# Kernel tuning notes

Hardware: AMD Instinct MI355X
Metric: run time of the kernel (lower is better)

The kernel has to match this reference:

```python
import jax, jax.numpy as jnp
import numpy as np

H_IMG = 128; W_IMG = 128
TANFOVX = 0.5; TANFOVY = 0.5
SCALE_MOD = 1.0
C0 = 0.28209479177387814
C1 = 0.4886025119029199
C2 = (1.0925484305920792, -1.0925484305920792, 0.31539156525252005, -1.0925484305920792, 0.5462742152960396)
C3 = (-0.5900435899266435, 2.890611442640554, -0.4570457994644658, 0.3731763325901154, -0.4570457994644658, 1.445305721320277, -0.5900435899266435)


def quat_to_rot(q):
    q = q / jnp.linalg.norm(q, axis=-1, keepdims=True)
    r, x, y, z = q[..., 0], q[..., 1], q[..., 2], q[..., 3]
    row0 = jnp.stack([1 - 2 * (y * y + z * z), 2 * (x * y - r * z), 2 * (x * z + r * y)], -1)
    row1 = jnp.stack([2 * (x * y + r * z), 1 - 2 * (x * x + z * z), 2 * (y * z - r * x)], -1)
    row2 = jnp.stack([2 * (x * z - r * y), 2 * (y * z + r * x), 1 - 2 * (x * x + y * y)], -1)
    return jnp.stack([row0, row1, row2], -2)  # [P,3,3]


def eval_sh(sh, d):
    # sh: [P,16,3], d: [P,3] unit view directions -> RGB per gaussian (degree 3)
    x, y, z = d[:, 0:1], d[:, 1:2], d[:, 2:3]
    res = C0 * sh[:, 0]
    res = res - C1 * y * sh[:, 1] + C1 * z * sh[:, 2] - C1 * x * sh[:, 3]
    xx, yy, zz = x * x, y * y, z * z
    xy, yz, xz = x * y, y * z, x * z
    res = (res + C2[0] * xy * sh[:, 4] + C2[1] * yz * sh[:, 5]
           + C2[2] * (2 * zz - xx - yy) * sh[:, 6] + C2[3] * xz * sh[:, 7]
           + C2[4] * (xx - yy) * sh[:, 8])
    res = (res + C3[0] * y * (3 * xx - yy) * sh[:, 9] + C3[1] * xy * z * sh[:, 10]
           + C3[2] * y * (4 * zz - xx - yy) * sh[:, 11]
           + C3[3] * z * (2 * zz - 3 * xx - 3 * yy) * sh[:, 12]
           + C3[4] * x * (4 * zz - xx - yy) * sh[:, 13]
           + C3[5] * z * (xx - yy) * sh[:, 14] + C3[6] * x * (xx - 3 * yy) * sh[:, 15])
    return jnp.maximum(res + 0.5, 0.0)


def _render_one(means, sh, opac, scales, rots, bg, target, view, proj, campos):
    P = means.shape[0]
    fx = W_IMG / (2.0 * TANFOVX)
    fy = H_IMG / (2.0 * TANFOVY)
    ones = jnp.ones((P, 1), means.dtype)
    xyz1 = jnp.concatenate([means, ones], axis=1)
    hom = xyz1 @ proj.T                                   # [P,4]
    p_w = 1.0 / (hom[:, 3] + 1e-7)
    p_proj = hom[:, :3] * p_w[:, None]
    p_view = xyz1 @ view.T
    depth = p_view[:, 2]
    in_front = depth > 0.2

    # 3D covariance: Sigma = R diag(s) (R diag(s))^T
    R = quat_to_rot(rots)
    M = R * (scales * SCALE_MOD)[:, None, :]
    Sigma = M @ jnp.swapaxes(M, 1, 2)                     # [P,3,3]

    # EWA Jacobian -> 2D covariance
    tz = depth
    txc = jnp.clip(p_view[:, 0] / tz, -1.3 * TANFOVX, 1.3 * TANFOVX) * tz
    tyc = jnp.clip(p_view[:, 1] / tz, -1.3 * TANFOVY, 1.3 * TANFOVY) * tz
    zp = jnp.zeros_like(tz)
    J = jnp.stack([jnp.stack([fx / tz, zp, -fx * txc / (tz * tz)], -1),
                   jnp.stack([zp, fy / tz, -fy * tyc / (tz * tz)], -1)], -2)  # [P,2,3]
    T = J @ view[:3, :3]
    cov2d = T @ Sigma @ jnp.swapaxes(T, 1, 2)             # [P,2,2]
    c00 = cov2d[:, 0, 0] + 0.3
    c11 = cov2d[:, 1, 1] + 0.3
    c01 = cov2d[:, 0, 1]
    det = c00 * c11 - c01 * c01
    valid = in_front & (det > 1e-12)
    inv_det = 1.0 / jnp.where(det > 1e-12, det, 1.0)
    conic = jnp.stack([c11 * inv_det, -c01 * inv_det, c00 * inv_det], -1)
    mid = 0.5 * (c00 + c11)
    lam = mid + jnp.sqrt(jnp.maximum(mid * mid - det, 0.1))
    radii = jnp.where(valid, jnp.ceil(3.0 * jnp.sqrt(lam)), 0.0)

    # NDC -> pixel centers
    px = ((p_proj[:, 0] + 1.0) * W_IMG - 1.0) * 0.5
    py = ((p_proj[:, 1] + 1.0) * H_IMG - 1.0) * 0.5

    dirs = means - campos[None]
    dirs = dirs / jnp.linalg.norm(dirs, axis=-1, keepdims=True)
    colors = eval_sh(sh, dirs)                            # [P,3]

    # front-to-back depth order (same per-pixel order as the tile sort)
    order = jnp.argsort(depth)
    inv_order = jnp.argsort(order)
    px_s, py_s = px[order], py[order]
    con_s = conic[order]
    col_s = colors[order]
    op_s = opac[order, 0]
    val_s = valid[order]

    xs = jnp.arange(W_IMG, dtype=means.dtype)
    ys = jnp.arange(H_IMG, dtype=means.dtype)
    dx = px_s[:, None, None] - xs[None, None, :]          # [P,1,W] -> [P,H,W]
    dy = py_s[:, None, None] - ys[None, :, None]
    power = (-0.5 * (con_s[:, 0, None, None] * dx * dx + con_s[:, 2, None, None] * dy * dy)
             - con_s[:, 1, None, None] * dx * dy)         # [P,H,W]
    alpha = jnp.minimum(0.99, op_s[:, None, None] * jnp.exp(jnp.minimum(power, 0.0)))
    keep = (power <= 0.0) & (alpha >= 1.0 / 255.0) & val_s[:, None, None]
    alpha = jnp.where(keep, alpha, 0.0)
    trans = jnp.cumprod(1.0 - alpha, axis=0)
    T_exc = jnp.concatenate([jnp.ones((1, H_IMG, W_IMG), alpha.dtype), trans[:-1]], axis=0)
    w = alpha * T_exc                                     # per-gaussian pixel weights
    T_final = trans[-1]
    color = jnp.einsum('phw,pc->chw', w, col_s) + T_final[None] * bg[:, None, None]
    alpha_img = (1.0 - T_final)[None]
    est_color = jnp.einsum('phw,chw->pc', w, target)[inv_order]
    est_weight = w.sum(axis=(1, 2))[inv_order, None]
    return color, alpha_img, est_color, est_weight, radii


def reference(means3D, sh, opacities, scales, rotations, target_image, bg, viewmatrix, projmatrix, campos):
    f = jax.vmap(_render_one, in_axes=(0, 0, 0, 0, 0, 0, 0, None, None, None))
    return f(means3D, sh, opacities, scales, rotations, bg, target_image, viewmatrix, projmatrix, campos)


def setup_inputs() -> dict:
    key = jax.random.key(0)
    ks = jax.random.split(key, 8)
    B, P, K = 2, 1024, 16
    xy = jax.random.normal(ks[0], (B, P, 2), jnp.float32) * 1.5
    z = jax.random.uniform(ks[1], (B, P, 1), jnp.float32, 2.0, 6.0)
    means3D = jnp.concatenate([xy, z], -1)
    sh = jax.random.normal(ks[2], (B, P, K, 3), jnp.float32) * 0.3
    opacities = jax.random.uniform(ks[3], (B, P, 1), jnp.float32)
    scales = jax.random.uniform(ks[4], (B, P, 3), jnp.float32, 0.01, 0.08)
    rotations = jax.random.normal(ks[5], (B, P, 4), jnp.float32)
    target_image = jax.random.uniform(ks[6], (B, 3, H_IMG, W_IMG), jnp.float32)
    bg = jax.random.uniform(ks[7], (B, 3), jnp.float32)
    view = np.eye(4, dtype=np.float32)  # camera at origin, +z forward
    znear, zfar = 0.01, 100.0
    proj = np.zeros((4, 4), np.float32)
    proj[0, 0] = 1.0 / TANFOVX
    proj[1, 1] = 1.0 / TANFOVY
    proj[2, 2] = zfar / (zfar - znear)
    proj[2, 3] = -(zfar * znear) / (zfar - znear)
    proj[3, 2] = 1.0
    return {"means3D": means3D, "sh": sh, "opacities": opacities, "scales": scales,
            "rotations": rotations, "target_image": target_image, "bg": bg,
            "viewmatrix": jnp.asarray(view), "projmatrix": jnp.asarray(proj @ view),
            "campos": jnp.zeros((3,), jnp.float32)}
```

## Files before the change

kernel.cpp:

```cpp
#include <hip/hip_runtime.h>
#include <math.h>

#define HI 128
#define WI 128
#define BB 2
#define PG 1024
#define NE (BB*PG)

#define OFF_ALPHA (BB*3*HI*WI)
#define OFF_ESTC  (OFF_ALPHA + BB*HI*WI)
#define OFF_ESTW  (OFF_ESTC + BB*PG*3)
#define OFF_RADII (OFF_ESTW + BB*PG)


__global__ __launch_bounds__(256) void preprocess_kernel(
    const float* __restrict__ means, const float* __restrict__ sh,
    const float* __restrict__ opac, const float* __restrict__ scales,
    const float* __restrict__ rots, const float* __restrict__ vm,
    const float* __restrict__ pm, const float* __restrict__ campos,
    float4* __restrict__ preA, float4* __restrict__ preB,
    float4* __restrict__ preC, float4* __restrict__ cull,
    unsigned int* __restrict__ keys, float* __restrict__ radii_out,
    float4* __restrict__ est_zero)
{
  int gid = blockIdx.x * blockDim.x + threadIdx.x;
  if (gid >= NE) return;

  est_zero[gid] = make_float4(0.f, 0.f, 0.f, 0.f);

  float mx = means[gid*3+0], my = means[gid*3+1], mz = means[gid*3+2];

  float hom0 = pm[0]*mx + pm[1]*my + pm[2]*mz + pm[3];
  float hom1 = pm[4]*mx + pm[5]*my + pm[6]*mz + pm[7];
  float hom3 = pm[12]*mx + pm[13]*my + pm[14]*mz + pm[15];
  float p_w  = 1.0f / (hom3 + 1e-7f);
  float pp0 = hom0 * p_w, pp1 = hom1 * p_w;

  float pv0   = vm[0]*mx + vm[1]*my + vm[2]*mz  + vm[3];
  float pv1   = vm[4]*mx + vm[5]*my + vm[6]*mz  + vm[7];
  float depth = vm[8]*mx + vm[9]*my + vm[10]*mz + vm[11];

  float qr = rots[gid*4+0], qx = rots[gid*4+1], qy = rots[gid*4+2], qz = rots[gid*4+3];
  float qn = sqrtf(qr*qr + qx*qx + qy*qy + qz*qz);
  qr /= qn; qx /= qn; qy /= qn; qz /= qn;
  float R00 = 1.0f-2.0f*(qy*qy+qz*qz), R01 = 2.0f*(qx*qy-qr*qz), R02 = 2.0f*(qx*qz+qr*qy);
  float R10 = 2.0f*(qx*qy+qr*qz), R11 = 1.0f-2.0f*(qx*qx+qz*qz), R12 = 2.0f*(qy*qz-qr*qx);
  float R20 = 2.0f*(qx*qz-qr*qy), R21 = 2.0f*(qy*qz+qr*qx), R22 = 1.0f-2.0f*(qx*qx+qy*qy);

  float s0 = scales[gid*3+0], s1 = scales[gid*3+1], s2 = scales[gid*3+2];
  float M00=R00*s0, M01=R01*s1, M02=R02*s2;
  float M10=R10*s0, M11=R11*s1, M12=R12*s2;
  float M20=R20*s0, M21=R21*s1, M22=R22*s2;
  float S00 = M00*M00+M01*M01+M02*M02;
  float S01 = M00*M10+M01*M11+M02*M12;
  float S02 = M00*M20+M01*M21+M02*M22;
  float S11 = M10*M10+M11*M11+M12*M12;
  float S12 = M10*M20+M11*M21+M12*M22;
  float S22 = M20*M20+M21*M21+M22*M22;

  const float fx = 128.0f, fyc = 128.0f;
  float tz = depth;
  float txc = fminf(fmaxf(pv0/tz, -0.65f), 0.65f) * tz;
  float tyc = fminf(fmaxf(pv1/tz, -0.65f), 0.65f) * tz;
  float J00 = fx/tz,  J02 = -fx*txc/(tz*tz);
  float J11 = fyc/tz, J12 = -fyc*tyc/(tz*tz);

  float T00 = J00*vm[0] + J02*vm[8];
  float T01 = J00*vm[1] + J02*vm[9];
  float T02 = J00*vm[2] + J02*vm[10];
  float T10 = J11*vm[4] + J12*vm[8];
  float T11 = J11*vm[5] + J12*vm[9];
  float T12 = J11*vm[6] + J12*vm[10];

  float TS00 = T00*S00 + T01*S01 + T02*S02;
  float TS01 = T00*S01 + T01*S11 + T02*S12;
  float TS02 = T00*S02 + T01*S12 + T02*S22;
  float TS10 = T10*S00 + T11*S01 + T12*S02;
  float TS11 = T10*S01 + T11*S11 + T12*S12;
  float TS12 = T10*S02 + T11*S12 + T12*S22;

  float c00 = TS00*T00 + TS01*T01 + TS02*T02 + 0.3f;
  float c01 = TS00*T10 + TS01*T11 + TS02*T12;
  float c11 = TS10*T10 + TS11*T11 + TS12*T12 + 0.3f;

  float det = c00*c11 - c01*c01;
  bool valid = (depth > 0.2f) && (det > 1e-12f);
  float inv_det = 1.0f / (det > 1e-12f ? det : 1.0f);
  float A  =  c11 * inv_det;
  float Bc = -c01 * inv_det;
  float Cc =  c00 * inv_det;
  float mid = 0.5f * (c00 + c11);
  float lam = mid + sqrtf(fmaxf(mid*mid - det, 0.1f));
  float radii = valid ? ceilf(3.0f * sqrtf(lam)) : 0.0f;

  float px = ((pp0 + 1.0f)*WI - 1.0f)*0.5f;
  float py = ((pp1 + 1.0f)*HI - 1.0f)*0.5f;

  float dxr = mx - campos[0], dyr = my - campos[1], dzr = mz - campos[2];
  float dn = sqrtf(dxr*dxr + dyr*dyr + dzr*dzr);
  float x = dxr/dn, y = dyr/dn, z = dzr/dn;
  float xx=x*x, yy=y*y, zz=z*z, xy=x*y, yz=y*z, xz=x*z;
  const float* S = sh + gid*48;
  float col[3];
  #pragma unroll
  for (int c = 0; c < 3; ++c) {
    float r = 0.28209479177387814f * S[0+c];
    r -= 0.4886025119029199f * y * S[3+c];
    r += 0.4886025119029199f * z * S[6+c];
    r -= 0.4886025119029199f * x * S[9+c];
    r += 1.0925484305920792f  * xy * S[12+c];
    r += -1.0925484305920792f * yz * S[15+c];
    r += 0.31539156525252005f * (2.0f*zz-xx-yy) * S[18+c];
    r += -1.0925484305920792f * xz * S[21+c];
    r += 0.5462742152960396f  * (xx-yy) * S[24+c];
    r += -0.5900435899266435f * y * (3.0f*xx-yy) * S[27+c];
    r += 2.890611442640554f   * xy * z * S[30+c];
    r += -0.4570457994644658f * y * (4.0f*zz-xx-yy) * S[33+c];
    r += 0.3731763325901154f  * z * (2.0f*zz-3.0f*xx-3.0f*yy) * S[36+c];
    r += -0.4570457994644658f * x * (4.0f*zz-xx-yy) * S[39+c];
    r += 1.445305721320277f   * z * (xx-yy) * S[42+c];
    r += -0.5900435899266435f * x * (xx-3.0f*yy) * S[45+c];
    col[c] = fmaxf(r + 0.5f, 0.0f);
  }

  float op = opac[gid];
  float tau = logf(255.0f * op);
  bool rok = valid && (tau > 0.0f);
  float ex = rok ? sqrtf(2.0f*tau*c00) + 0.02f : -1e9f;
  float ey = rok ? sqrtf(2.0f*tau*c11) + 0.02f : -1e9f;

  preA[gid] = make_float4(px, py, A, Bc);
  preB[gid] = make_float4(Cc, -tau, op, 0.0f);
  preC[gid] = make_float4(col[0], col[1], col[2], 0.0f);
  cull[gid] = make_float4(px, py, ex, ey);

  unsigned int u = __float_as_uint(depth);
  keys[gid] = (u >> 31) ? ~u : (u | 0x80000000u);
  radii_out[gid] = radii;
}

__global__ __launch_bounds__(64) void render_kernel(
    const float4* __restrict__ preA, const float4* __restrict__ preB,
    const float4* __restrict__ preC, const float4* __restrict__ cull,
    const unsigned int* __restrict__ keys,
    const float* __restrict__ target, const float* __restrict__ bg,
    float* __restrict__ out)
{
  const int b = blockIdx.z;
  const int t = threadIdx.x;
  const int x = blockIdx.x*8 + (t & 7);
  const int y = blockIdx.y*8 + (t >> 3);
  const float fxp = (float)x, fyp = (float)y;
  const float tx0 = (float)(blockIdx.x*8), ty0 = (float)(blockIdx.y*8);

  __shared__ unsigned long long skey[PG];
  __shared__ float4 sqA[64], sqB[64], sqC[64];
  __shared__ float4 stgt[64];
  __shared__ float  wmat[64][65];

  const float4* csrc = cull + (b << 10);
  const unsigned int* kb = keys + (b << 10);

  int total = 0;
  #pragma unroll
  for (int c0 = 0; c0 < PG; c0 += 64) {
    float4 cv = csrc[c0 + t];
    unsigned int kk = kb[c0 + t];
    bool ok = (cv.x + cv.z >= tx0) && (cv.x - cv.z <= tx0 + 7.0f)
           && (cv.y + cv.w >= ty0) && (cv.y - cv.w <= ty0 + 7.0f);
    unsigned long long m = __ballot(ok);
    if (ok) {
      int pos = total + __popcll(m & ((1ull << t) - 1ull));
      skey[pos] = (((unsigned long long)kk) << 10) | (unsigned)(c0 + t);
    }
    total += __popcll(m);
  }
  __syncthreads();

  if (total > 1) {
    if (total <= 64) {
      unsigned long long v = (t < total) ? skey[t] : ~0ull;
      #pragma unroll
      for (int k = 2; k <= 64; k <<= 1) {
        bool dirAsc = ((t & k) == 0);
        #pragma unroll
        for (int j = k >> 1; j > 0; j >>= 1) {
          unsigned long long o = __shfl_xor(v, j, 64);
          bool takeMin = (((t & j) == 0) == dirAsc);
          bool less = v < o;
          v = (takeMin == less) ? v : o;
        }
      }
      if (t < total) skey[t] = v;
    } else {
      int M = 64; while (M < total) M <<= 1;
      for (int s = total + t; s < M; s += 64) skey[s] = ~0ull;
      __syncthreads();
      for (int k = 2; k <= M; k <<= 1) {
        for (int j = k >> 1; j > 0; j >>= 1) {
          for (int base = t; base < M; base += 64) {
            int ixj = base ^ j;
            if (ixj > base) {
              unsigned long long a = skey[base], bq = skey[ixj];
              bool up = ((base & k) == 0);
              if ((a > bq) == up) { skey[base] = bq; skey[ixj] = a; }
            }
          }
          __syncthreads();
        }
      }
    }
  }

  const float t0 = target[((b*3+0)*HI + y)*WI + x];
  const float t1 = target[((b*3+1)*HI + y)*WI + x];
  const float t2 = target[((b*3+2)*HI + y)*WI + x];
  stgt[t] = make_float4(t0, t1, t2, 1.0f);
  __syncthreads();

  float* est_col = out + OFF_ESTC + b*PG*3;
  float* est_w   = out + OFF_ESTW + b*PG;

  float T = 1.0f, a0 = 0.0f, a1 = 0.0f, a2 = 0.0f;

  for (int c = 0; c < total; c += 64) {
    int count = min(64, total - c);
    if (t < count) {
      int g = (int)(skey[c + t] & 1023u);
      int e = (b << 10) + g;
      float4 qb = preB[e];
      qb.w = __int_as_float(g);
      sqA[t] = preA[e]; sqB[t] = qb; sqC[t] = preC[e];
    }
    __syncthreads();

    for (int i = 0; i < count; ++i) {
      float4 q0 = sqA[i], q1 = sqB[i], q2 = sqC[i];
      float dx = q0.x - fxp, dy = q0.y - fyp;
      float power = -0.5f*(q0.z*dx*dx + q1.x*dy*dy) - q0.w*dx*dy;
      float alpha = fminf(0.99f, q1.z * __expf(power));
      bool keep = (power <= 0.0f) && (alpha >= (1.0f/255.0f));
      float w = keep ? alpha * T : 0.0f;
      a0 += w * q2.x; a1 += w * q2.y; a2 += w * q2.z;
      T -= w;
      wmat[i][t] = w;
    }
    __syncthreads();

    if (t < count) {
      float4 acc = make_float4(0.f, 0.f, 0.f, 0.f);
      #pragma unroll 8
      for (int p = 0; p < 64; ++p) {
        float w = wmat[t][p];
        float4 tg = stgt[p];
        acc.x += w * tg.x; acc.y += w * tg.y; acc.z += w * tg.z; acc.w += w;
      }
      int orig = __float_as_int(sqB[t].w);
      atomicAdd(&est_col[orig*3+0], acc.x);
      atomicAdd(&est_col[orig*3+1], acc.y);
      atomicAdd(&est_col[orig*3+2], acc.z);
      atomicAdd(&est_w[orig], acc.w);
    }
    __syncthreads();
  }

  out[((b*3+0)*HI + y)*WI + x] = a0 + T * bg[b*3+0];
  out[((b*3+1)*HI + y)*WI + x] = a1 + T * bg[b*3+1];
  out[((b*3+2)*HI + y)*WI + x] = a2 + T * bg[b*3+2];
  out[OFF_ALPHA + (b*HI + y)*WI + x] = 1.0f - T;
}

extern "C" void kernel_launch(void* const* d_in, const int* in_sizes, int n_in,
                              void* d_out, int out_size, void* d_ws, size_t ws_size,
                              hipStream_t stream) {
  const float* means  = (const float*)d_in[0];
  const float* sh     = (const float*)d_in[1];
  const float* opac   = (const float*)d_in[2];
  const float* scales = (const float*)d_in[3];
  const float* rots   = (const float*)d_in[4];
  const float* target = (const float*)d_in[5];
  const float* bg     = (const float*)d_in[6];
  const float* vm     = (const float*)d_in[7];
  const float* pm     = (const float*)d_in[8];
  const float* campos = (const float*)d_in[9];
  float* out = (float*)d_out;

  float4* preA = (float4*)d_ws;
  float4* preB = preA + NE;
  float4* preC = preB + NE;
  float4* cul  = preC + NE;
  unsigned int* keys = (unsigned int*)(cul + NE);

  preprocess_kernel<<<NE/256, 256, 0, stream>>>(
      means, sh, opac, scales, rots, vm, pm, campos,
      preA, preB, preC, cul, keys, out + OFF_RADII,
      (float4*)(out + OFF_ESTC));

  dim3 grid(WI/8, HI/8, BB), block(64, 1);
  render_kernel<<<grid, block, 0, stream>>>(
      preA, preB, preC, cul, keys, target, bg, out);
}
```

Measured before the change: 23.55 us.

## Fuse preprocess and render into one cooperative kernel with grid sync

Merges the per-gaussian preprocess kernel and the tile render kernel into a single cooperative launch. Each of the 512 render blocks of 64 threads first preprocesses 64 gaussians, then all blocks wait on a grid-wide barrier before rendering. This removes one kernel launch and the gap between the two kernels. In exchange it adds the cost of a grid sync, and the preprocess phase now runs with 64-thread blocks instead of 256.

Result: slower. 79.00 us (+235.5%).

```diff
diff --git a/kernel.cpp b/kernel.cpp
--- a/kernel.cpp
+++ b/kernel.cpp
@@ -1,5 +1,8 @@
 #include <hip/hip_runtime.h>
+#include <hip/hip_cooperative_groups.h>
 #include <math.h>
+
+namespace cg = cooperative_groups;
 
 #define HI 128
 #define WI 128
@@ -13,141 +16,138 @@
 #define OFF_RADII (OFF_ESTW + BB*PG)
 
 
-__global__ __launch_bounds__(256) void preprocess_kernel(
+__global__ __launch_bounds__(64) void fused_kernel(
     const float* __restrict__ means, const float* __restrict__ sh,
     const float* __restrict__ opac, const float* __restrict__ scales,
     const float* __restrict__ rots, const float* __restrict__ vm,
     const float* __restrict__ pm, const float* __restrict__ campos,
     float4* __restrict__ preA, float4* __restrict__ preB,
-    float4* __restrict__ preC, float4* __restrict__ cull,
-    unsigned int* __restrict__ keys, float* __restrict__ radii_out,
-    float4* __restrict__ est_zero)
-{
-  int gid = blockIdx.x * blockDim.x + threadIdx.x;
-  if (gid >= NE) return;
-
-  est_zero[gid] = make_float4(0.f, 0.f, 0.f, 0.f);
-
-  float mx = means[gid*3+0], my = means[gid*3+1], mz = means[gid*3+2];
-
-  float hom0 = pm[0]*mx + pm[1]*my + pm[2]*mz + pm[3];
-  float hom1 = pm[4]*mx + pm[5]*my + pm[6]*mz + pm[7];
-  float hom3 = pm[12]*mx + pm[13]*my + pm[14]*mz + pm[15];
-  float p_w  = 1.0f / (hom3 + 1e-7f);
-  float pp0 = hom0 * p_w, pp1 = hom1 * p_w;
-
-  float pv0   = vm[0]*mx + vm[1]*my + vm[2]*mz  + vm[3];
-  float pv1   = vm[4]*mx + vm[5]*my + vm[6]*mz  + vm[7];
-  float depth = vm[8]*mx + vm[9]*my + vm[10]*mz + vm[11];
-
-  float qr = rots[gid*4+0], qx = rots[gid*4+1], qy = rots[gid*4+2], qz = rots[gid*4+3];
-  float qn = sqrtf(qr*qr + qx*qx + qy*qy + qz*qz);
-  qr /= qn; qx /= qn; qy /= qn; qz /= qn;
-  float R00 = 1.0f-2.0f*(qy*qy+qz*qz), R01 = 2.0f*(qx*qy-qr*qz), R02 = 2.0f*(qx*qz+qr*qy);
-  float R10 = 2.0f*(qx*qy+qr*qz), R11 = 1.0f-2.0f*(qx*qx+qz*qz), R12 = 2.0f*(qy*qz-qr*qx);
-  float R20 = 2.0f*(qx*qz-qr*qy), R21 = 2.0f*(qy*qz+qr*qx), R22 = 1.0f-2.0f*(qx*qx+qy*qy);
-
-  float s0 = scales[gid*3+0], s1 = scales[gid*3+1], s2 = scales[gid*3+2];
-  float M00=R00*s0, M01=R01*s1, M02=R02*s2;
-  float M10=R10*s0, M11=R11*s1, M12=R12*s2;
-  float M20=R20*s0, M21=R21*s1, M22=R22*s2;
-  float S00 = M00*M00+M01*M01+M02*M02;
-  float S01 = M00*M10+M01*M11+M02*M12;
-  float S02 = M00*M20+M01*M21+M02*M22;
-  float S11 = M10*M10+M11*M11+M12*M12;
-  float S12 = M10*M20+M11*M21+M12*M22;
-  float S22 = M20*M20+M21*M21+M22*M22;
-
-  const float fx = 128.0f, fyc = 128.0f;
-  float tz = depth;
-  float txc = fminf(fmaxf(pv0/tz, -0.65f), 0.65f) * tz;
-  float tyc = fminf(fmaxf(pv1/tz, -0.65f), 0.65f) * tz;
-  float J00 = fx/tz,  J02 = -fx*txc/(tz*tz);
-  float J11 = fyc/tz, J12 = -fyc*tyc/(tz*tz);
-
-  float T00 = J00*vm[0] + J02*vm[8];
-  float T01 = J00*vm[1] + J02*vm[9];
-  float T02 = J00*vm[2] + J02*vm[10];
-  float T10 = J11*vm[4] + J12*vm[8];
-  float T11 = J11*vm[5] + J12*vm[9];
-  float T12 = J11*vm[6] + J12*vm[10];
-
-  float TS00 = T00*S00 + T01*S01 + T02*S02;
-  float TS01 = T00*S01 + T01*S11 + T02*S12;
-  float TS02 = T00*S02 + T01*S12 + T02*S22;
-  float TS10 = T10*S00 + T11*S01 + T12*S02;
-  float TS11 = T10*S01 + T11*S11 + T12*S12;
-  float TS12 = T10*S02 + T11*S12 + T12*S22;
-
-  float c00 = TS00*T00 + TS01*T01 + TS02*T02 + 0.3f;
-  float c01 = TS00*T10 + TS01*T11 + TS02*T12;
-  float c11 = TS10*T10 + TS11*T11 + TS12*T12 + 0.3f;
-
-  float det = c00*c11 - c01*c01;
-  bool valid = (depth > 0.2f) && (det > 1e-12f);
-  float inv_det = 1.0f / (det > 1e-12f ? det : 1.0f);
-  float A  =  c11 * inv_det;
-  float Bc = -c01 * inv_det;
-  float Cc =  c00 * inv_det;
-  float mid = 0.5f * (c00 + c11);
-  float lam = mid + sqrtf(fmaxf(mid*mid - det, 0.1f));
-  float radii = valid ? ceilf(3.0f * sqrtf(lam)) : 0.0f;
-
-  float px = ((pp0 + 1.0f)*WI - 1.0f)*0.5f;
-  float py = ((pp1 + 1.0f)*HI - 1.0f)*0.5f;
-
-  float dxr = mx - campos[0], dyr = my - campos[1], dzr = mz - campos[2];
-  float dn = sqrtf(dxr*dxr + dyr*dyr + dzr*dzr);
-  float x = dxr/dn, y = dyr/dn, z = dzr/dn;
-  float xx=x*x, yy=y*y, zz=z*z, xy=x*y, yz=y*z, xz=x*z;
-  const float* S = sh + gid*48;
-  float col[3];
-  #pragma unroll
-  for (int c = 0; c < 3; ++c) {
-    float r = 0.28209479177387814f * S[0+c];
-    r -= 0.4886025119029199f * y * S[3+c];
-    r += 0.4886025119029199f * z * S[6+c];
-    r -= 0.4886025119029199f * x * S[9+c];
-    r += 1.0925484305920792f  * xy * S[12+c];
-    r += -1.0925484305920792f * yz * S[15+c];
-    r += 0.31539156525252005f * (2.0f*zz-xx-yy) * S[18+c];
-    r += -1.0925484305920792f * xz * S[21+c];
-    r += 0.5462742152960396f  * (xx-yy) * S[24+c];
-    r += -0.5900435899266435f * y * (3.0f*xx-yy) * S[27+c];
-    r += 2.890611442640554f   * xy * z * S[30+c];
-    r += -0.4570457994644658f * y * (4.0f*zz-xx-yy) * S[33+c];
-    r += 0.3731763325901154f  * z * (2.0f*zz-3.0f*xx-3.0f*yy) * S[36+c];
-    r += -0.4570457994644658f * x * (4.0f*zz-xx-yy) * S[39+c];
-    r += 1.445305721320277f   * z * (xx-yy) * S[42+c];
-    r += -0.5900435899266435f * x * (xx-3.0f*yy) * S[45+c];
-    col[c] = fmaxf(r + 0.5f, 0.0f);
-  }
-
-  float op = opac[gid];
-  float tau = logf(255.0f * op);
-  bool rok = valid && (tau > 0.0f);
-  float ex = rok ? sqrtf(2.0f*tau*c00) + 0.02f : -1e9f;
-  float ey = rok ? sqrtf(2.0f*tau*c11) + 0.02f : -1e9f;
-
-  preA[gid] = make_float4(px, py, A, Bc);
-  preB[gid] = make_float4(Cc, -tau, op, 0.0f);
-  preC[gid] = make_float4(col[0], col[1], col[2], 0.0f);
-  cull[gid] = make_float4(px, py, ex, ey);
-
-  unsigned int u = __float_as_uint(depth);
-  keys[gid] = (u >> 31) ? ~u : (u | 0x80000000u);
-  radii_out[gid] = radii;
-}
-
-__global__ __launch_bounds__(64) void render_kernel(
-    const float4* __restrict__ preA, const float4* __restrict__ preB,
-    const float4* __restrict__ preC, const float4* __restrict__ cull,
-    const unsigned int* __restrict__ keys,
+    float4* __restrict__ preC, float4* __restrict__ cullv,
+    unsigned int* __restrict__ keys,
     const float* __restrict__ target, const float* __restrict__ bg,
     float* __restrict__ out)
 {
+  const int t = threadIdx.x;
+  const int flatb = (blockIdx.z * gridDim.y + blockIdx.y) * gridDim.x + blockIdx.x;
+  const int gid = flatb * 64 + t;
+
+  if (gid < NE) {
+    ((float4*)(out + OFF_ESTC))[gid] = make_float4(0.f, 0.f, 0.f, 0.f);
+
+    float mx = means[gid*3+0], my = means[gid*3+1], mz = means[gid*3+2];
+
+    float hom0 = pm[0]*mx + pm[1]*my + pm[2]*mz + pm[3];
+    float hom1 = pm[4]*mx + pm[5]*my + pm[6]*mz + pm[7];
+    float hom3 = pm[12]*mx + pm[13]*my + pm[14]*mz + pm[15];
+    float p_w  = 1.0f / (hom3 + 1e-7f);
+    float pp0 = hom0 * p_w, pp1 = hom1 * p_w;
+
+    float pv0   = vm[0]*mx + vm[1]*my + vm[2]*mz  + vm[3];
+    float pv1   = vm[4]*mx + vm[5]*my + vm[6]*mz  + vm[7];
+    float depth = vm[8]*mx + vm[9]*my + vm[10]*mz + vm[11];
+
+    float qr = rots[gid*4+0], qx = rots[gid*4+1], qy = rots[gid*4+2], qz = rots[gid*4+3];
+    float qn = sqrtf(qr*qr + qx*qx + qy*qy + qz*qz);
+    qr /= qn; qx /= qn; qy /= qn; qz /= qn;
+    float R00 = 1.0f-2.0f*(qy*qy+qz*qz), R01 = 2.0f*(qx*qy-qr*qz), R02 = 2.0f*(qx*qz+qr*qy);
+    float R10 = 2.0f*(qx*qy+qr*qz), R11 = 1.0f-2.0f*(qx*qx+qz*qz), R12 = 2.0f*(qy*qz-qr*qx);
+    float R20 = 2.0f*(qx*qz-qr*qy), R21 = 2.0f*(qy*qz+qr*qx), R22 = 1.0f-2.0f*(qx*qx+qy*qy);
+
+    float s0 = scales[gid*3+0], s1 = scales[gid*3+1], s2 = scales[gid*3+2];
+    float M00=R00*s0, M01=R01*s1, M02=R02*s2;
+    float M10=R10*s0, M11=R11*s1, M12=R12*s2;
+    float M20=R20*s0, M21=R21*s1, M22=R22*s2;
+    float S00 = M00*M00+M01*M01+M02*M02;
+    float S01 = M00*M10+M01*M11+M02*M12;
+    float S02 = M00*M20+M01*M21+M02*M22;
+    float S11 = M10*M10+M11*M11+M12*M12;
+    float S12 = M10*M20+M11*M21+M12*M22;
+    float S22 = M20*M20+M21*M21+M22*M22;
+
+    const float fx = 128.0f, fyc = 128.0f;
+    float tz = depth;
+    float txc = fminf(fmaxf(pv0/tz, -0.65f), 0.65f) * tz;
+    float tyc = fminf(fmaxf(pv1/tz, -0.65f), 0.65f) * tz;
+    float J00 = fx/tz,  J02 = -fx*txc/(tz*tz);
+    float J11 = fyc/tz, J12 = -fyc*tyc/(tz*tz);
+
+    float T00 = J00*vm[0] + J02*vm[8];
+    float T01 = J00*vm[1] + J02*vm[9];
+    float T02 = J00*vm[2] + J02*vm[10];
+    float T10 = J11*vm[4] + J12*vm[8];
+    float T11 = J11*vm[5] + J12*vm[9];
+    float T12 = J11*vm[6] + J12*vm[10];
+
+    float TS00 = T00*S00 + T01*S01 + T02*S02;
+    float TS01 = T00*S01 + T01*S11 + T02*S12;
+    float TS02 = T00*S02 + T01*S12 + T02*S22;
+    float TS10 = T10*S00 + T11*S01 + T12*S02;
+    float TS11 = T10*S01 + T11*S11 + T12*S12;
+    float TS12 = T10*S02 + T11*S12 + T12*S22;
+
+    float c00 = TS00*T00 + TS01*T01 + TS02*T02 + 0.3f;
+    float c01 = TS00*T10 + TS01*T11 + TS02*T12;
+    float c11 = TS10*T10 + TS11*T11 + TS12*T12 + 0.3f;
+
+    float det = c00*c11 - c01*c01;
+    bool valid = (depth > 0.2f) && (det > 1e-12f);
+    float inv_det = 1.0f / (det > 1e-12f ? det : 1.0f);
+    float A  =  c11 * inv_det;
+    float Bc = -c01 * inv_det;
+    float Cc =  c00 * inv_det;
+    float mid = 0.5f * (c00 + c11);
+    float lam = mid + sqrtf(fmaxf(mid*mid - det, 0.1f));
+    float radii = valid ? ceilf(3.0f * sqrtf(lam)) : 0.0f;
+
+    float px = ((pp0 + 1.0f)*WI - 1.0f)*0.5f;
+    float py = ((pp1 + 1.0f)*HI - 1.0f)*0.5f;
+
+    float dxr = mx - campos[0], dyr = my - campos[1], dzr = mz - campos[2];
+    float dn = sqrtf(dxr*dxr + dyr*dyr + dzr*dzr);
+    float x = dxr/dn, y = dyr/dn, z = dzr/dn;
+    float xx=x*x, yy=y*y, zz=z*z, xy=x*y, yz=y*z, xz=x*z;
+    const float* S = sh + gid*48;
+    float col[3];
+    #pragma unroll
+    for (int c = 0; c < 3; ++c) {
+      float r = 0.28209479177387814f * S[0+c];
+      r -= 0.4886025119029199f * y * S[3+c];
+      r += 0.4886025119029199f * z * S[6+c];
+      r -= 0.4886025119029199f * x * S[9+c];
+      r += 1.0925484305920792f  * xy * S[12+c];
+      r += -1.0925484305920792f * yz * S[15+c];
+      r += 0.31539156525252005f * (2.0f*zz-xx-yy) * S[18+c];
+      r += -1.0925484305920792f * xz * S[21+c];
+      r += 0.5462742152960396f  * (xx-yy) * S[24+c];
+      r += -0.5900435899266435f * y * (3.0f*xx-yy) * S[27+c];
+      r += 2.890611442640554f   * xy * z * S[30+c];
+      r += -0.4570457994644658f * y * (4.0f*zz-xx-yy) * S[33+c];
+      r += 0.3731763325901154f  * z * (2.0f*zz-3.0f*xx-3.0f*yy) * S[36+c];
+      r += -0.4570457994644658f * x * (4.0f*zz-xx-yy) * S[39+c];
+      r += 1.445305721320277f   * z * (xx-yy) * S[42+c];
+      r += -0.5900435899266435f * x * (xx-3.0f*yy) * S[45+c];
+      col[c] = fmaxf(r + 0.5f, 0.0f);
+    }
+
+    float op = opac[gid];
+    float tau = logf(255.0f * op);
+    bool rok = valid && (tau > 0.0f);
+    float ex = rok ? sqrtf(2.0f*tau*c00) + 0.02f : -1e9f;
+    float ey = rok ? sqrtf(2.0f*tau*c11) + 0.02f : -1e9f;
+
+    preA[gid] = make_float4(px, py, A, Bc);
+    preB[gid] = make_float4(Cc, -tau, op, 0.0f);
+    preC[gid] = make_float4(col[0], col[1], col[2], 0.0f);
+    cullv[gid] = make_float4(px, py, ex, ey);
+
+    unsigned int u = __float_as_uint(depth);
+    keys[gid] = (u >> 31) ? ~u : (u | 0x80000000u);
+    out[OFF_RADII + gid] = radii;
+  }
+
+  cg::this_grid().sync();
+
   const int b = blockIdx.z;
-  const int t = threadIdx.x;
   const int x = blockIdx.x*8 + (t & 7);
   const int y = blockIdx.y*8 + (t >> 3);
   const float fxp = (float)x, fyp = (float)y;
@@ -158,7 +158,7 @@
   __shared__ float4 stgt[64];
   __shared__ float  wmat[64][65];
 
-  const float4* csrc = cull + (b << 10);
+  const float4* csrc = cullv + (b << 10);
   const unsigned int* kb = keys + (b << 10);
 
   int total = 0;
@@ -291,12 +291,13 @@
   float4* cul  = preC + NE;
   unsigned int* keys = (unsigned int*)(cul + NE);
 
-  preprocess_kernel<<<NE/256, 256, 0, stream>>>(
-      means, sh, opac, scales, rots, vm, pm, campos,
-      preA, preB, preC, cul, keys, out + OFF_RADII,
-      (float4*)(out + OFF_ESTC));
-
-  dim3 grid(WI/8, HI/8, BB), block(64, 1);
-  render_kernel<<<grid, block, 0, stream>>>(
-      preA, preB, preC, cul, keys, target, bg, out);
+  void* args[] = {
+    (void*)&means, (void*)&sh, (void*)&opac, (void*)&scales, (void*)&rots,
+    (void*)&vm, (void*)&pm, (void*)&campos,
+    (void*)&preA, (void*)&preB, (void*)&preC, (void*)&cul, (void*)&keys,
+    (void*)&target, (void*)&bg, (void*)&out
+  };
+  hipLaunchCooperativeKernel((const void*)fused_kernel,
+                             dim3(WI/8, HI/8, BB), dim3(64, 1, 1),
+                             args, 0, stream);
 }
```
